# Kernel optimization log

Measured on AMD Instinct MI355X. Metric: run time of the kernel, lower is better.

Reference implementation:

```python
import jax, jax.numpy as jnp
import numpy as np

B, I, H = 64, 1024, 1024
WSCALE = 0.02  # approx Xavier std for 1024-dim fan-in/out


def setup_inputs() -> dict:
    key = jax.random.key(0)
    ks = jax.random.split(key, 9)
    return {
        "input": jax.random.normal(ks[0], (B, I), jnp.float32),
        "h": jax.random.normal(ks[1], (B, H), jnp.float32),
        "C": jax.random.normal(ks[2], (B, H, H), jnp.float32),
        "weight_ih": jax.random.normal(ks[3], (3 * H, I), jnp.float32) * WSCALE,
        "weight_hh": jax.random.normal(ks[4], (3 * H, H), jnp.float32) * WSCALE,
        "bias": jnp.zeros((3 * H,), jnp.float32),
        "Wq_w": jax.random.normal(ks[5], (H, I), jnp.float32) * WSCALE,
        "Wq_b": jnp.zeros((H,), jnp.float32),
        "Wk_w": jax.random.normal(ks[6], (H, I), jnp.float32) * WSCALE,
        "Wk_b": jnp.zeros((H,), jnp.float32),
        "Wv_w": jax.random.normal(ks[7], (H, I), jnp.float32) * WSCALE,
        "Wv_b": jnp.zeros((H,), jnp.float32),
    }


def reference(input, h, C, weight_ih, weight_hh, bias, Wq_w, Wq_b, Wk_w, Wk_b, Wv_w, Wv_b):
    # gates: [B, 3H]
    gates = input @ weight_ih.T + bias + h @ weight_hh.T
    i, f, o = jnp.split(gates, 3, axis=1)
    i = jnp.exp(i)
    f = jnp.exp(f)
    o = jax.nn.sigmoid(o)
    q = input @ Wq_w.T + Wq_b
    k = input @ Wk_w.T + Wk_b
    v = input @ Wv_w.T + Wv_b
    # matrix memory update: outer product v k^T gated by i, decay by f (broadcast over columns)
    C_new = f[:, :, None] * C + i[:, :, None] * (v[:, :, None] * k[:, None, :])
    # readout: h = o * (q^T C_new), contracting q over the row (v) axis of C
    h_new = o * jnp.einsum("bi,bij->bj", q, C_new)
    return (h_new, C_new)
```

## Files before the change

kernel.cpp:

```cpp
#include <hip/hip_runtime.h>
#include <math.h>

typedef float v4 __attribute__((ext_vector_type(4)));

#define HD 1024
#define NB 64
#define NCHUNK 16

#define WS_XT      0
#define WS_HT      65536
#define WS_IGT     131072
#define WS_FGT     196608
#define WS_QT      262144
#define WS_VT      327680
#define WS_OGN     393216
#define WS_KN      458752
#define WS_PART    524288

__global__ __launch_bounds__(256) void k_transpose(const float* __restrict__ input,
                                                   const float* __restrict__ h,
                                                   float* __restrict__ ws) {
    int g = blockIdx.x * 256 + threadIdx.x;
    int which = g >> 14;
    int idx = g & 16383;
    int kk = idx >> 6;
    int b  = idx & 63;
    const float* src = which ? h : input;
    v4 val = *(const v4*)(src + (size_t)b * HD + kk * 4);
    v4* dst = (v4*)(ws + (which ? WS_HT : WS_XT));
    dst[kk * 64 + b] = val;
}

__global__ __launch_bounds__(256) void k_gemm(
    const float* __restrict__ Wih, const float* __restrict__ Whh, const float* __restrict__ bias,
    const float* __restrict__ Wq, const float* __restrict__ Wqb,
    const float* __restrict__ Wk, const float* __restrict__ Wkb,
    const float* __restrict__ Wv, const float* __restrict__ Wvb,
    float* __restrict__ ws) {
    const v4* Xt = (const v4*)(ws + WS_XT);
    const v4* Ht = (const v4*)(ws + WS_HT);
    int lane = threadIdx.x & 63;
    int wid  = __builtin_amdgcn_readfirstlane(threadIdx.x >> 6);
    int blk  = blockIdx.x;

    if (blk < 768) {
        int r = blk * 4 + wid;
        const v4* wr1 = (const v4*)(Wih + (size_t)r * HD);
        const v4* wr2 = (const v4*)(Whh + (size_t)r * HD);
        float acc = 0.f;
        for (int kk = 0; kk < 256; ++kk) {
            v4 w = wr1[kk];
            v4 x = Xt[kk * 64 + lane];
            acc += w.x * x.x + w.y * x.y + w.z * x.z + w.w * x.w;
        }
        for (int kk = 0; kk < 256; ++kk) {
            v4 w = wr2[kk];
            v4 x = Ht[kk * 64 + lane];
            acc += w.x * x.x + w.y * x.y + w.z * x.z + w.w * x.w;
        }
        acc += bias[r];
        if (r < 1024) {
            ws[WS_IGT + r * 64 + lane] = expf(acc);
        } else if (r < 2048) {
            ws[WS_FGT + (r - 1024) * 64 + lane] = expf(acc);
        } else {
            float o = 1.f / (1.f + expf(-acc));
            ws[WS_OGN + lane * HD + (r - 2048)] = o;
        }
    } else {
        int r2 = (blk - 768) * 4 + wid;
        int sel = r2 >> 10;
        int rr  = r2 & 1023;
        const float* W  = (sel == 0) ? Wq  : (sel == 1) ? Wk  : Wv;
        const float* Bv = (sel == 0) ? Wqb : (sel == 1) ? Wkb : Wvb;
        const v4* wr = (const v4*)(W + (size_t)rr * HD);
        float acc = 0.f;
        for (int kk = 0; kk < 256; ++kk) {
            v4 w = wr[kk];
            v4 x = Xt[kk * 64 + lane];
            acc += w.x * x.x + w.y * x.y + w.z * x.z + w.w * x.w;
        }
        acc += Bv[rr];
        if (sel == 0)      ws[WS_QT + rr * 64 + lane] = acc;
        else if (sel == 1) ws[WS_KN + lane * HD + rr] = acc;
        else               ws[WS_VT + rr * 64 + lane] = acc;
    }
}

__global__ __launch_bounds__(256) void k_update(const float* __restrict__ C,
                                                float* __restrict__ out,
                                                float* __restrict__ ws) {
    int b  = blockIdx.x >> 4;
    int c  = blockIdx.x & 15;
    int i0 = c << 6;
    int tid = threadIdx.x;

    __shared__ float fg_s[64], iv_s[64], q_s[64];
    if (tid < 64) {
        int i = i0 + tid;
        fg_s[tid] = ws[WS_FGT + i * 64 + b];
        iv_s[tid] = ws[WS_IGT + i * 64 + b] * ws[WS_VT + i * 64 + b];
        q_s[tid]  = ws[WS_QT + i * 64 + b];
    }
    __syncthreads();

    v4 k4 = *(const v4*)(ws + WS_KN + b * HD + tid * 4);
    const v4* Cb = (const v4*)(C + (size_t)b * HD * HD) + tid;
    v4*       On = (v4*)(out + NB * HD + (size_t)b * HD * HD) + tid;
    v4 acc = {0.f, 0.f, 0.f, 0.f};

    for (int ii = 0; ii < 64; ++ii) {
        int i = i0 + ii;
        v4 c4 = __builtin_nontemporal_load(&Cb[(size_t)i * 256]);
        float fi = fg_s[ii], ivi = iv_s[ii], qi = q_s[ii];
        v4 cn;
        cn.x = fi * c4.x + ivi * k4.x;
        cn.y = fi * c4.y + ivi * k4.y;
        cn.z = fi * c4.z + ivi * k4.z;
        cn.w = fi * c4.w + ivi * k4.w;
        __builtin_nontemporal_store(cn, &On[(size_t)i * 256]);
        acc.x += qi * cn.x;
        acc.y += qi * cn.y;
        acc.z += qi * cn.z;
        acc.w += qi * cn.w;
    }
    *(v4*)(ws + WS_PART + (size_t)(c * 64 + b) * HD + tid * 4) = acc;
}

__global__ __launch_bounds__(256) void k_final(float* __restrict__ out,
                                               const float* __restrict__ ws) {
    int b = blockIdx.x;
    int tid = threadIdx.x;
    const v4* part = (const v4*)(ws + WS_PART);
    v4 s = {0.f, 0.f, 0.f, 0.f};
    for (int c = 0; c < NCHUNK; ++c) {
        v4 p = part[(size_t)(c * 64 + b) * 256 + tid];
        s.x += p.x; s.y += p.y; s.z += p.z; s.w += p.w;
    }
    v4 o4 = *(const v4*)(ws + WS_OGN + b * HD + tid * 4);
    v4 r;
    r.x = o4.x * s.x; r.y = o4.y * s.y; r.z = o4.z * s.z; r.w = o4.w * s.w;
    *(v4*)(out + b * HD + tid * 4) = r;
}

extern "C" void kernel_launch(void* const* d_in, const int* in_sizes, int n_in,
                              void* d_out, int out_size, void* d_ws, size_t ws_size,
                              hipStream_t stream) {
    const float* input = (const float*)d_in[0];
    const float* h     = (const float*)d_in[1];
    const float* C     = (const float*)d_in[2];
    const float* Wih   = (const float*)d_in[3];
    const float* Whh   = (const float*)d_in[4];
    const float* bias  = (const float*)d_in[5];
    const float* Wq_w  = (const float*)d_in[6];
    const float* Wq_b  = (const float*)d_in[7];
    const float* Wk_w  = (const float*)d_in[8];
    const float* Wk_b  = (const float*)d_in[9];
    const float* Wv_w  = (const float*)d_in[10];
    const float* Wv_b  = (const float*)d_in[11];
    float* out = (float*)d_out;
    float* ws  = (float*)d_ws;

    k_transpose<<<128, 256, 0, stream>>>(input, h, ws);
    k_gemm<<<1536, 256, 0, stream>>>(Wih, Whh, bias, Wq_w, Wq_b, Wk_w, Wk_b, Wv_w, Wv_b, ws);
    k_update<<<1024, 256, 0, stream>>>(C, out, ws);
    k_final<<<64, 256, 0, stream>>>(out, ws);
}
```

Baseline: 542.8 us.

## Register-block GEMM over four weight rows per wave and unroll update loop

The gate/QKV GEMM now computes four output rows per wave, so each transposed activation vector load is reused across four weight rows. The block size drops to 128 threads with half as many blocks, and the O and K outputs use vector stores. The C update loop is unrolled by four with two accumulators to raise memory-level parallelism. In exchange, each wave reads weight rows with a strided access pattern and register pressure goes up.

```diff
diff --git a/kernel.cpp b/kernel.cpp
--- a/kernel.cpp
+++ b/kernel.cpp
@@ -31,7 +31,7 @@
     dst[kk * 64 + b] = val;
 }
 
-__global__ __launch_bounds__(256) void k_gemm(
+__global__ __launch_bounds__(128) void k_gemm(
     const float* __restrict__ Wih, const float* __restrict__ Whh, const float* __restrict__ bias,
     const float* __restrict__ Wq, const float* __restrict__ Wqb,
     const float* __restrict__ Wk, const float* __restrict__ Wkb,
@@ -43,47 +43,98 @@
     int wid  = __builtin_amdgcn_readfirstlane(threadIdx.x >> 6);
     int blk  = blockIdx.x;
 
-    if (blk < 768) {
-        int r = blk * 4 + wid;
-        const v4* wr1 = (const v4*)(Wih + (size_t)r * HD);
-        const v4* wr2 = (const v4*)(Whh + (size_t)r * HD);
-        float acc = 0.f;
+    if (blk < 384) {
+        int r0 = blk * 8 + wid * 4;
+        const v4* w1 = (const v4*)(Wih + (size_t)r0 * HD);
+        const v4* w2 = (const v4*)(Whh + (size_t)r0 * HD);
+        float a0 = 0.f, a1 = 0.f, a2 = 0.f, a3 = 0.f;
+        #pragma unroll 4
         for (int kk = 0; kk < 256; ++kk) {
-            v4 w = wr1[kk];
-            v4 x = Xt[kk * 64 + lane];
-            acc += w.x * x.x + w.y * x.y + w.z * x.z + w.w * x.w;
-        }
+            v4 x  = Xt[kk * 64 + lane];
+            v4 p0 = w1[kk];
+            v4 p1 = w1[kk + 256];
+            v4 p2 = w1[kk + 512];
+            v4 p3 = w1[kk + 768];
+            a0 += p0.x * x.x + p0.y * x.y + p0.z * x.z + p0.w * x.w;
+            a1 += p1.x * x.x + p1.y * x.y + p1.z * x.z + p1.w * x.w;
+            a2 += p2.x * x.x + p2.y * x.y + p2.z * x.z + p2.w * x.w;
+            a3 += p3.x * x.x + p3.y * x.y + p3.z * x.z + p3.w * x.w;
+        }
+        #pragma unroll 4
         for (int kk = 0; kk < 256; ++kk) {
-            v4 w = wr2[kk];
-            v4 x = Ht[kk * 64 + lane];
-            acc += w.x * x.x + w.y * x.y + w.z * x.z + w.w * x.w;
-        }
-        acc += bias[r];
-        if (r < 1024) {
-            ws[WS_IGT + r * 64 + lane] = expf(acc);
-        } else if (r < 2048) {
-            ws[WS_FGT + (r - 1024) * 64 + lane] = expf(acc);
+            v4 x  = Ht[kk * 64 + lane];
+            v4 p0 = w2[kk];
+            v4 p1 = w2[kk + 256];
+            v4 p2 = w2[kk + 512];
+            v4 p3 = w2[kk + 768];
+            a0 += p0.x * x.x + p0.y * x.y + p0.z * x.z + p0.w * x.w;
+            a1 += p1.x * x.x + p1.y * x.y + p1.z * x.z + p1.w * x.w;
+            a2 += p2.x * x.x + p2.y * x.y + p2.z * x.z + p2.w * x.w;
+            a3 += p3.x * x.x + p3.y * x.y + p3.z * x.z + p3.w * x.w;
+        }
+        a0 += bias[r0 + 0];
+        a1 += bias[r0 + 1];
+        a2 += bias[r0 + 2];
+        a3 += bias[r0 + 3];
+        int seg = r0 >> 10;
+        if (seg == 0) {
+            ws[WS_IGT + (r0 + 0) * 64 + lane] = expf(a0);
+            ws[WS_IGT + (r0 + 1) * 64 + lane] = expf(a1);
+            ws[WS_IGT + (r0 + 2) * 64 + lane] = expf(a2);
+            ws[WS_IGT + (r0 + 3) * 64 + lane] = expf(a3);
+        } else if (seg == 1) {
+            int rr = r0 - 1024;
+            ws[WS_FGT + (rr + 0) * 64 + lane] = expf(a0);
+            ws[WS_FGT + (rr + 1) * 64 + lane] = expf(a1);
+            ws[WS_FGT + (rr + 2) * 64 + lane] = expf(a2);
+            ws[WS_FGT + (rr + 3) * 64 + lane] = expf(a3);
         } else {
-            float o = 1.f / (1.f + expf(-acc));
-            ws[WS_OGN + lane * HD + (r - 2048)] = o;
+            int rr = r0 - 2048;
+            v4 o;
+            o.x = 1.f / (1.f + expf(-a0));
+            o.y = 1.f / (1.f + expf(-a1));
+            o.z = 1.f / (1.f + expf(-a2));
+            o.w = 1.f / (1.f + expf(-a3));
+            *(v4*)(ws + WS_OGN + lane * HD + rr) = o;
         }
     } else {
-        int r2 = (blk - 768) * 4 + wid;
+        int r2  = (blk - 384) * 8 + wid * 4;
         int sel = r2 >> 10;
         int rr  = r2 & 1023;
         const float* W  = (sel == 0) ? Wq  : (sel == 1) ? Wk  : Wv;
         const float* Bv = (sel == 0) ? Wqb : (sel == 1) ? Wkb : Wvb;
         const v4* wr = (const v4*)(W + (size_t)rr * HD);
-        float acc = 0.f;
+        float a0 = 0.f, a1 = 0.f, a2 = 0.f, a3 = 0.f;
+        #pragma unroll 4
         for (int kk = 0; kk < 256; ++kk) {
-            v4 w = wr[kk];
-            v4 x = Xt[kk * 64 + lane];
-            acc += w.x * x.x + w.y * x.y + w.z * x.z + w.w * x.w;
-        }
-        acc += Bv[rr];
-        if (sel == 0)      ws[WS_QT + rr * 64 + lane] = acc;
-        else if (sel == 1) ws[WS_KN + lane * HD + rr] = acc;
-        else               ws[WS_VT + rr * 64 + lane] = acc;
+            v4 x  = Xt[kk * 64 + lane];
+            v4 p0 = wr[kk];
+            v4 p1 = wr[kk + 256];
+            v4 p2 = wr[kk + 512];
+            v4 p3 = wr[kk + 768];
+            a0 += p0.x * x.x + p0.y * x.y + p0.z * x.z + p0.w * x.w;
+            a1 += p1.x * x.x + p1.y * x.y + p1.z * x.z + p1.w * x.w;
+            a2 += p2.x * x.x + p2.y * x.y + p2.z * x.z + p2.w * x.w;
+            a3 += p3.x * x.x + p3.y * x.y + p3.z * x.z + p3.w * x.w;
+        }
+        a0 += Bv[rr + 0];
+        a1 += Bv[rr + 1];
+        a2 += Bv[rr + 2];
+        a3 += Bv[rr + 3];
+        if (sel == 0) {
+            ws[WS_QT + (rr + 0) * 64 + lane] = a0;
+            ws[WS_QT + (rr + 1) * 64 + lane] = a1;
+            ws[WS_QT + (rr + 2) * 64 + lane] = a2;
+            ws[WS_QT + (rr + 3) * 64 + lane] = a3;
+        } else if (sel == 1) {
+            v4 kv; kv.x = a0; kv.y = a1; kv.z = a2; kv.w = a3;
+            *(v4*)(ws + WS_KN + lane * HD + rr) = kv;
+        } else {
+            ws[WS_VT + (rr + 0) * 64 + lane] = a0;
+            ws[WS_VT + (rr + 1) * 64 + lane] = a1;
+            ws[WS_VT + (rr + 2) * 64 + lane] = a2;
+            ws[WS_VT + (rr + 3) * 64 + lane] = a3;
+        }
     }
 }
 
@@ -107,23 +158,44 @@
     v4 k4 = *(const v4*)(ws + WS_KN + b * HD + tid * 4);
     const v4* Cb = (const v4*)(C + (size_t)b * HD * HD) + tid;
     v4*       On = (v4*)(out + NB * HD + (size_t)b * HD * HD) + tid;
-    v4 acc = {0.f, 0.f, 0.f, 0.f};
-
-    for (int ii = 0; ii < 64; ++ii) {
-        int i = i0 + ii;
-        v4 c4 = __builtin_nontemporal_load(&Cb[(size_t)i * 256]);
-        float fi = fg_s[ii], ivi = iv_s[ii], qi = q_s[ii];
-        v4 cn;
-        cn.x = fi * c4.x + ivi * k4.x;
-        cn.y = fi * c4.y + ivi * k4.y;
-        cn.z = fi * c4.z + ivi * k4.z;
-        cn.w = fi * c4.w + ivi * k4.w;
-        __builtin_nontemporal_store(cn, &On[(size_t)i * 256]);
-        acc.x += qi * cn.x;
-        acc.y += qi * cn.y;
-        acc.z += qi * cn.z;
-        acc.w += qi * cn.w;
-    }
+    v4 acc0 = {0.f, 0.f, 0.f, 0.f};
+    v4 acc1 = {0.f, 0.f, 0.f, 0.f};
+
+    for (int ii = 0; ii < 64; ii += 4) {
+        size_t r0 = (size_t)(i0 + ii) * 256;
+        v4 c0 = __builtin_nontemporal_load(&Cb[r0]);
+        v4 c1 = __builtin_nontemporal_load(&Cb[r0 + 256]);
+        v4 c2 = __builtin_nontemporal_load(&Cb[r0 + 512]);
+        v4 c3 = __builtin_nontemporal_load(&Cb[r0 + 768]);
+
+        float f0 = fg_s[ii + 0], g0 = iv_s[ii + 0], q0 = q_s[ii + 0];
+        float f1 = fg_s[ii + 1], g1 = iv_s[ii + 1], q1 = q_s[ii + 1];
+        float f2 = fg_s[ii + 2], g2 = iv_s[ii + 2], q2 = q_s[ii + 2];
+        float f3 = fg_s[ii + 3], g3 = iv_s[ii + 3], q3 = q_s[ii + 3];
+
+        v4 n0, n1, n2, n3;
+        n0.x = f0 * c0.x + g0 * k4.x; n0.y = f0 * c0.y + g0 * k4.y;
+        n0.z = f0 * c0.z + g0 * k4.z; n0.w = f0 * c0.w + g0 * k4.w;
+        n1.x = f1 * c1.x + g1 * k4.x; n1.y = f1 * c1.y + g1 * k4.y;
+        n1.z = f1 * c1.z + g1 * k4.z; n1.w = f1 * c1.w + g1 * k4.w;
+        n2.x = f2 * c2.x + g2 * k4.x; n2.y = f2 * c2.y + g2 * k4.y;
+        n2.z = f2 * c2.z + g2 * k4.z; n2.w = f2 * c2.w + g2 * k4.w;
+        n3.x = f3 * c3.x + g3 * k4.x; n3.y = f3 * c3.y + g3 * k4.y;
+        n3.z = f3 * c3.z + g3 * k4.z; n3.w = f3 * c3.w + g3 * k4.w;
+
+        __builtin_nontemporal_store(n0, &On[r0]);
+        __builtin_nontemporal_store(n1, &On[r0 + 256]);
+        __builtin_nontemporal_store(n2, &On[r0 + 512]);
+        __builtin_nontemporal_store(n3, &On[r0 + 768]);
+
+        acc0.x += q0 * n0.x; acc0.y += q0 * n0.y; acc0.z += q0 * n0.z; acc0.w += q0 * n0.w;
+        acc1.x += q1 * n1.x; acc1.y += q1 * n1.y; acc1.z += q1 * n1.z; acc1.w += q1 * n1.w;
+        acc0.x += q2 * n2.x; acc0.y += q2 * n2.y; acc0.z += q2 * n2.z; acc0.w += q2 * n2.w;
+        acc1.x += q3 * n3.x; acc1.y += q3 * n3.y; acc1.z += q3 * n3.z; acc1.w += q3 * n3.w;
+    }
+    v4 acc;
+    acc.x = acc0.x + acc1.x; acc.y = acc0.y + acc1.y;
+    acc.z = acc0.z + acc1.z; acc.w = acc0.w + acc1.w;
     *(v4*)(ws + WS_PART + (size_t)(c * 64 + b) * HD + tid * 4) = acc;
 }
 
@@ -162,7 +234,7 @@
     float* ws  = (float*)d_ws;
 
     k_transpose<<<128, 256, 0, stream>>>(input, h, ws);
-    k_gemm<<<1536, 256, 0, stream>>>(Wih, Whh, bias, Wq_w, Wq_b, Wk_w, Wk_b, Wv_w, Wv_b, ws);
+    k_gemm<<<768, 128, 0, stream>>>(Wih, Whh, bias, Wq_w, Wq_b, Wk_w, Wk_b, Wv_w, Wv_b, ws);
     k_update<<<1024, 256, 0, stream>>>(C, out, ws);
     k_final<<<64, 256, 0, stream>>>(out, ws);
 }
```

Measured after the change: 609.7 us. 1.12x slower.

## Replace fp32 gate/projection GEMVs with bf16 MFMA split-K GEMM

Applied to the files above, without the earlier changes.

The scalar fp32 dot-product gate and QKV projection kernel is replaced by three stages. A prep kernel converts weights and inputs to bf16 in an MFMA-friendly packed layout. An MFMA kernel computes split-K partial tiles with 16x16x32 bf16 instructions. An activation kernel reduces the partials, adds biases and applies exp and sigmoid. This moves the small GEMMs onto matrix cores, at the cost of converting the weights to bf16 on every call, extra workspace traffic for the partials, and reduced precision that feeds into exp gates.

```diff
diff --git a/kernel.cpp b/kernel.cpp
--- a/kernel.cpp
+++ b/kernel.cpp
@@ -2,13 +2,15 @@
 #include <math.h>
 
 typedef float v4 __attribute__((ext_vector_type(4)));
+typedef float f32x4 __attribute__((ext_vector_type(4)));
+typedef __bf16 bf16x8 __attribute__((ext_vector_type(8)));
+typedef unsigned short u16;
+typedef unsigned short u16x8 __attribute__((ext_vector_type(8)));
 
 #define HD 1024
 #define NB 64
 #define NCHUNK 16
 
-#define WS_XT      0
-#define WS_HT      65536
 #define WS_IGT     131072
 #define WS_FGT     196608
 #define WS_QT      262144
@@ -16,74 +18,144 @@
 #define WS_OGN     393216
 #define WS_KN      458752
 #define WS_PART    524288
-
-__global__ __launch_bounds__(256) void k_transpose(const float* __restrict__ input,
-                                                   const float* __restrict__ h,
-                                                   float* __restrict__ ws) {
+#define WS_BPK     1572864
+#define WS_WPK     1638400
+#define WPK_QGRP   786432
+#define WS_PG      6356992
+#define WS_PQ      9502720
+
+static __device__ __forceinline__ u16 f2bf(float f) {
+    unsigned u = __float_as_uint(f);
+    u += 0x7FFFu + ((u >> 16) & 1u);
+    return (u16)(u >> 16);
+}
+
+__global__ __launch_bounds__(256) void k_prep(
+    const float* __restrict__ input, const float* __restrict__ h,
+    const float* __restrict__ Wih, const float* __restrict__ Whh,
+    const float* __restrict__ Wq, const float* __restrict__ Wk, const float* __restrict__ Wv,
+    float* __restrict__ ws) {
+    u16* wpk = (u16*)(ws + WS_WPK);
+    u16* bpk = (u16*)(ws + WS_BPK);
     int g = blockIdx.x * 256 + threadIdx.x;
-    int which = g >> 14;
-    int idx = g & 16383;
-    int kk = idx >> 6;
-    int b  = idx & 63;
-    const float* src = which ? h : input;
-    v4 val = *(const v4*)(src + (size_t)b * HD + kk * 4);
-    v4* dst = (v4*)(ws + (which ? WS_HT : WS_XT));
-    dst[kk * 64 + b] = val;
-}
-
-__global__ __launch_bounds__(256) void k_gemm(
-    const float* __restrict__ Wih, const float* __restrict__ Whh, const float* __restrict__ bias,
-    const float* __restrict__ Wq, const float* __restrict__ Wqb,
-    const float* __restrict__ Wk, const float* __restrict__ Wkb,
-    const float* __restrict__ Wv, const float* __restrict__ Wvb,
+
+    if (g < 1179648) {
+        const float* src;
+        size_t dst;
+        if (g < 393216) {
+            int r = g >> 7, k8 = g & 127;
+            src = Wih + (size_t)r * HD + k8 * 8;
+            int t = r >> 4, ks = k8 >> 2;
+            dst = ((size_t)(t * 64 + ks) * 64 + (((k8 & 3) << 4) | (r & 15))) * 8;
+        } else if (g < 786432) {
+            int gi = g - 393216;
+            int r = gi >> 7, k8 = gi & 127;
+            src = Whh + (size_t)r * HD + k8 * 8;
+            int t = r >> 4, ks = 32 + (k8 >> 2);
+            dst = ((size_t)(t * 64 + ks) * 64 + (((k8 & 3) << 4) | (r & 15))) * 8;
+        } else {
+            int gi = g - 786432;
+            int r2 = gi >> 7, k8 = gi & 127;
+            int sel = r2 >> 10, rr = r2 & 1023;
+            const float* W = (sel == 0) ? Wq : (sel == 1) ? Wk : Wv;
+            src = W + (size_t)rr * HD + k8 * 8;
+            int t = r2 >> 4, ks = k8 >> 2;
+            dst = (size_t)WPK_QGRP * 8 + ((size_t)(t * 32 + ks) * 64 + (((k8 & 3) << 4) | (r2 & 15))) * 8;
+        }
+        v4 f0 = *(const v4*)src;
+        v4 f1 = *(const v4*)(src + 4);
+        u16x8 pk;
+        pk[0] = f2bf(f0.x); pk[1] = f2bf(f0.y); pk[2] = f2bf(f0.z); pk[3] = f2bf(f0.w);
+        pk[4] = f2bf(f1.x); pk[5] = f2bf(f1.y); pk[6] = f2bf(f1.z); pk[7] = f2bf(f1.w);
+        *(u16x8*)(wpk + dst) = pk;
+    } else {
+        int o = g - 1179648;
+        int l = o & 63, jj = (o >> 6) & 3, ks2 = o >> 8;
+        const float* srcm = (ks2 < 32) ? input : h;
+        const float* src = srcm + (size_t)(jj * 16 + (l & 15)) * HD + (ks2 & 31) * 32 + (l >> 4) * 8;
+        v4 f0 = *(const v4*)src;
+        v4 f1 = *(const v4*)(src + 4);
+        u16x8 pk;
+        pk[0] = f2bf(f0.x); pk[1] = f2bf(f0.y); pk[2] = f2bf(f0.z); pk[3] = f2bf(f0.w);
+        pk[4] = f2bf(f1.x); pk[5] = f2bf(f1.y); pk[6] = f2bf(f1.z); pk[7] = f2bf(f1.w);
+        *(u16x8*)(bpk + (size_t)o * 8) = pk;
+    }
+}
+
+__global__ __launch_bounds__(256) void k_mfma(float* __restrict__ ws) {
+    int lane = threadIdx.x & 63;
+    int w = blockIdx.x * 4 + (threadIdx.x >> 6);
+    const bf16x8* Wp = (const bf16x8*)(ws + WS_WPK);
+    const bf16x8* Bp = (const bf16x8*)(ws + WS_BPK);
+
+    size_t aBase;
+    int ks0;
+    float* pout;
+    if (w < 3072) {
+        int t = w >> 4, c = w & 15;
+        ks0 = c * 4;
+        aBase = (size_t)(t * 64 + ks0) * 64;
+        pout = ws + WS_PG + (size_t)(c * 192 + t) * 1024;
+    } else {
+        int w2 = w - 3072;
+        int t = w2 >> 3, c = w2 & 7;
+        ks0 = c * 4;
+        aBase = (size_t)WPK_QGRP + (size_t)(t * 32 + ks0) * 64;
+        pout = ws + WS_PQ + (size_t)(c * 192 + t) * 1024;
+    }
+
+    f32x4 a0 = {0.f, 0.f, 0.f, 0.f};
+    f32x4 a1 = a0, a2 = a0, a3 = a0;
+    #pragma unroll
+    for (int s = 0; s < 4; ++s) {
+        bf16x8 a = Wp[aBase + (size_t)s * 64 + lane];
+        int kb = (ks0 + s) * 4;
+        bf16x8 b0 = Bp[(size_t)(kb + 0) * 64 + lane];
+        bf16x8 b1 = Bp[(size_t)(kb + 1) * 64 + lane];
+        bf16x8 b2 = Bp[(size_t)(kb + 2) * 64 + lane];
+        bf16x8 b3 = Bp[(size_t)(kb + 3) * 64 + lane];
+        a0 = __builtin_amdgcn_mfma_f32_16x16x32_bf16(a, b0, a0, 0, 0, 0);
+        a1 = __builtin_amdgcn_mfma_f32_16x16x32_bf16(a, b1, a1, 0, 0, 0);
+        a2 = __builtin_amdgcn_mfma_f32_16x16x32_bf16(a, b2, a2, 0, 0, 0);
+        a3 = __builtin_amdgcn_mfma_f32_16x16x32_bf16(a, b3, a3, 0, 0, 0);
+    }
+    int rb = (lane >> 4) * 4, cb = lane & 15;
+    #pragma unroll
+    for (int q = 0; q < 4; ++q) {
+        pout[(rb + q) * 64 +  0 + cb] = a0[q];
+        pout[(rb + q) * 64 + 16 + cb] = a1[q];
+        pout[(rb + q) * 64 + 32 + cb] = a2[q];
+        pout[(rb + q) * 64 + 48 + cb] = a3[q];
+    }
+}
+
+__global__ __launch_bounds__(256) void k_act(
+    const float* __restrict__ bias,
+    const float* __restrict__ Wqb, const float* __restrict__ Wkb, const float* __restrict__ Wvb,
     float* __restrict__ ws) {
-    const v4* Xt = (const v4*)(ws + WS_XT);
-    const v4* Ht = (const v4*)(ws + WS_HT);
-    int lane = threadIdx.x & 63;
-    int wid  = __builtin_amdgcn_readfirstlane(threadIdx.x >> 6);
-    int blk  = blockIdx.x;
-
-    if (blk < 768) {
-        int r = blk * 4 + wid;
-        const v4* wr1 = (const v4*)(Wih + (size_t)r * HD);
-        const v4* wr2 = (const v4*)(Whh + (size_t)r * HD);
-        float acc = 0.f;
-        for (int kk = 0; kk < 256; ++kk) {
-            v4 w = wr1[kk];
-            v4 x = Xt[kk * 64 + lane];
-            acc += w.x * x.x + w.y * x.y + w.z * x.z + w.w * x.w;
-        }
-        for (int kk = 0; kk < 256; ++kk) {
-            v4 w = wr2[kk];
-            v4 x = Ht[kk * 64 + lane];
-            acc += w.x * x.x + w.y * x.y + w.z * x.z + w.w * x.w;
-        }
-        acc += bias[r];
-        if (r < 1024) {
-            ws[WS_IGT + r * 64 + lane] = expf(acc);
-        } else if (r < 2048) {
-            ws[WS_FGT + (r - 1024) * 64 + lane] = expf(acc);
-        } else {
-            float o = 1.f / (1.f + expf(-acc));
-            ws[WS_OGN + lane * HD + (r - 2048)] = o;
-        }
+    int g = blockIdx.x * 256 + threadIdx.x;
+    if (g < 196608) {
+        int r = g >> 6, b = g & 63;
+        int t = r >> 4, ro = r & 15;
+        const float* P = ws + WS_PG + ro * 64 + b;
+        float s = bias[r];
+        #pragma unroll
+        for (int c = 0; c < 16; ++c) s += P[(size_t)(c * 192 + t) * 1024];
+        if (r < 1024)       ws[WS_IGT + r * 64 + b] = expf(s);
+        else if (r < 2048)  ws[WS_FGT + (r - 1024) * 64 + b] = expf(s);
+        else                ws[WS_OGN + b * HD + (r - 2048)] = 1.f / (1.f + expf(-s));
     } else {
-        int r2 = (blk - 768) * 4 + wid;
-        int sel = r2 >> 10;
-        int rr  = r2 & 1023;
-        const float* W  = (sel == 0) ? Wq  : (sel == 1) ? Wk  : Wv;
-        const float* Bv = (sel == 0) ? Wqb : (sel == 1) ? Wkb : Wvb;
-        const v4* wr = (const v4*)(W + (size_t)rr * HD);
-        float acc = 0.f;
-        for (int kk = 0; kk < 256; ++kk) {
-            v4 w = wr[kk];
-            v4 x = Xt[kk * 64 + lane];
-            acc += w.x * x.x + w.y * x.y + w.z * x.z + w.w * x.w;
-        }
-        acc += Bv[rr];
-        if (sel == 0)      ws[WS_QT + rr * 64 + lane] = acc;
-        else if (sel == 1) ws[WS_KN + lane * HD + rr] = acc;
-        else               ws[WS_VT + rr * 64 + lane] = acc;
+        int e = g - 196608;
+        int r2 = e >> 6, b = e & 63;
+        int t = r2 >> 4, ro = r2 & 15;
+        int sel = r2 >> 10, rr = r2 & 1023;
+        const float* P = ws + WS_PQ + ro * 64 + b;
+        float s = ((sel == 0) ? Wqb : (sel == 1) ? Wkb : Wvb)[rr];
+        #pragma unroll
+        for (int c = 0; c < 8; ++c) s += P[(size_t)(c * 192 + t) * 1024];
+        if (sel == 0)      ws[WS_QT + rr * 64 + b] = s;
+        else if (sel == 1) ws[WS_KN + b * HD + rr] = s;
+        else               ws[WS_VT + rr * 64 + b] = s;
     }
 }
 
@@ -161,8 +233,9 @@
     float* out = (float*)d_out;
     float* ws  = (float*)d_ws;
 
-    k_transpose<<<128, 256, 0, stream>>>(input, h, ws);
-    k_gemm<<<1536, 256, 0, stream>>>(Wih, Whh, bias, Wq_w, Wq_b, Wk_w, Wk_b, Wv_w, Wv_b, ws);
+    k_prep<<<4672, 256, 0, stream>>>(input, h, Wih, Whh, Wq_w, Wk_w, Wv_w, ws);
+    k_mfma<<<1152, 256, 0, stream>>>(ws);
+    k_act<<<1536, 256, 0, stream>>>(bias, Wq_b, Wk_b, Wv_b, ws);
     k_update<<<1024, 256, 0, stream>>>(C, out, ws);
     k_final<<<64, 256, 0, stream>>>(out, ws);
 }
```

After: 503.4 us. -7.2%, faster.
